# Kernel optimization log

Hardware: AMD Instinct MI355X
Metric: run time of the kernel (lower is better)

The kernel has to match this reference:

```python
import jax, jax.numpy as jnp
import numpy as np

VOCAB = 32000
EMB = 512
T = 20  # sentence_max_length
B = 64


def setup_inputs() -> dict:
    key = jax.random.key(0)
    ks = jax.random.split(key, 8)
    features = jax.random.normal(ks[0], (B, EMB), dtype=jnp.float32)
    captions = jax.random.randint(ks[1], (B, T), 0, VOCAB)
    W_emb = jax.random.normal(ks[2], (VOCAB, EMB), dtype=jnp.float32) * 0.02
    W_out = jax.random.normal(ks[3], (VOCAB, EMB), dtype=jnp.float32) * 0.02
    b_out = jnp.zeros((VOCAB,), dtype=jnp.float32)
    # LSTM params (PyTorch layout: [4*H, in], gate order i, f, g, o)
    W_ih = jax.random.normal(ks[4], (4 * EMB, EMB), dtype=jnp.float32) * (1.0 / np.sqrt(EMB))
    W_hh = jax.random.normal(ks[5], (4 * EMB, EMB), dtype=jnp.float32) * (1.0 / np.sqrt(EMB))
    b_ih = jnp.zeros((4 * EMB,), dtype=jnp.float32)
    b_hh = jnp.zeros((4 * EMB,), dtype=jnp.float32)
    return {"features": features, "captions": captions, "W_emb": W_emb,
            "W_out": W_out, "b_out": b_out, "W_ih": W_ih, "W_hh": W_hh,
            "b_ih": b_ih, "b_hh": b_hh}


def _lstm_scan(emb_steps, h0, c0, W_ih, W_hh, b_ih, b_hh):
    # emb_steps: [T-1, B, E]; returns stacked hidden states [T-1, B, E]
    def cell(carry, x):
        h, c = carry
        gates = x @ W_ih.T + b_ih + h @ W_hh.T + b_hh  # [B, 4E]
        i, f, g, o = jnp.split(gates, 4, axis=-1)
        i, f, o = jax.nn.sigmoid(i), jax.nn.sigmoid(f), jax.nn.sigmoid(o)
        g = jnp.tanh(g)
        c = f * c + i * g
        h = o * jnp.tanh(c)
        return (h, c), h

    (_, _), hs = jax.lax.scan(cell, (h0, c0), emb_steps)
    return hs


def reference(features, captions, W_emb, W_out, b_out, W_ih, W_hh, b_ih, b_hh):
    # Teacher-forced decode. h0 = zeros, c0 = features (per original code).
    emb = W_emb[captions]  # [B, T, E]
    h0 = jnp.zeros_like(features)
    c0 = features
    # Step i (i=1..T-1) consumes embedding of captions[:, i-1]
    xs = jnp.swapaxes(emb[:, : T - 1], 0, 1)  # [T-1, B, E]
    hs = _lstm_scan(xs, h0, c0, W_ih, W_hh, b_ih, b_hh)  # [T-1, B, E]
    hs = jnp.swapaxes(hs, 0, 1)  # [B, T-1, E]
    # out[0] = Linear(Embed(captions[:,0])); out[i] = Linear(h_i)
    seq = jnp.concatenate([emb[:, :1], hs], axis=1)  # [B, T, E]
    logits = jnp.einsum("bte,ve->btv", seq, W_out) + b_out  # [B, T, V]
    return logits
```

## Files before the change

### kernel.cpp

```cpp
#include <hip/hip_runtime.h>
#include <hip/hip_bf16.h>

#define Bb 64
#define Tt 20
#define Ee 512
#define Vv 32000
#define NB 32

typedef __hip_bfloat16 bf16;
typedef __attribute__((ext_vector_type(8))) short bf16x8;
typedef __attribute__((ext_vector_type(4))) float f32x4;

__device__ __forceinline__ bf16 f2bf(float x) { return __float2bfloat16(x); }

__global__ void embed_init(const int* __restrict__ caps, const float* __restrict__ Wemb,
                           bf16* __restrict__ emb, bf16* __restrict__ seq,
                           unsigned int* __restrict__ bar) {
  int row = blockIdx.x;
  int t = row % Tt;
  int tid = threadIdx.x;
  if (row == 0) {
    for (int i = tid; i < NB * 16 + Tt; i += 128) bar[i] = 0;
  }
  int tok = caps[row];
  float4 v = ((const float4*)(Wemb + (size_t)tok * Ee))[tid];
  union { ushort4 u; bf16 h[4]; } pk;
  pk.h[0] = f2bf(v.x); pk.h[1] = f2bf(v.y); pk.h[2] = f2bf(v.z); pk.h[3] = f2bf(v.w);
  ((ushort4*)(emb + (size_t)row * Ee))[tid] = pk.u;
  if (t == 0) ((ushort4*)(seq + (size_t)row * Ee))[tid] = pk.u;
}

__global__ __launch_bounds__(256) void xproj(
    const bf16* __restrict__ A,
    const float* __restrict__ Bw,
    const float* __restrict__ bih, const float* __restrict__ bhh,
    float* __restrict__ gx)
{
  __shared__ __align__(16) bf16 As[128 * 64];
  __shared__ __align__(16) bf16 Bs[128 * 64];
  int tid = threadIdx.x;
  int lane = tid & 63;
  int quad = lane >> 4, ln = lane & 15;
  int wid = tid >> 6;
  int wm = wid & 1, wn = wid >> 1;
  int n0 = blockIdx.x * 128, m0 = blockIdx.y * 128;

  f32x4 zero = {0.f, 0.f, 0.f, 0.f};
  f32x4 acc[4][4];
#pragma unroll
  for (int mt = 0; mt < 4; ++mt)
#pragma unroll
    for (int nt = 0; nt < 4; ++nt) acc[mt][nt] = zero;

  for (int k0 = 0; k0 < Ee; k0 += 64) {
    uint4 avv[4];
    float4 bf0[4], bf1[4];
#pragma unroll
    for (int q = 0; q < 4; ++q) {
      int fb = (q * 256 + tid) * 16;
      int row = fb >> 7;
      int c8 = (fb & 127) >> 1;
      avv[q] = *(const uint4*)((const char*)A + ((size_t)(m0 + row) * Ee + k0) * 2 + (fb & 127));
      const float* src = Bw + (size_t)(n0 + row) * Ee + k0 + c8;
      bf0[q] = *(const float4*)(src);
      bf1[q] = *(const float4*)(src + 4);
    }
#pragma unroll
    for (int q = 0; q < 4; ++q) {
      int fb = (q * 256 + tid) * 16;
      *(uint4*)((char*)As + fb) = avv[q];
      union { uint4 u; bf16 h[8]; } pk;
      pk.h[0] = f2bf(bf0[q].x); pk.h[1] = f2bf(bf0[q].y);
      pk.h[2] = f2bf(bf0[q].z); pk.h[3] = f2bf(bf0[q].w);
      pk.h[4] = f2bf(bf1[q].x); pk.h[5] = f2bf(bf1[q].y);
      pk.h[6] = f2bf(bf1[q].z); pk.h[7] = f2bf(bf1[q].w);
      *(uint4*)((char*)Bs + fb) = pk.u;
    }
    __syncthreads();

#pragma unroll
    for (int kk = 0; kk < 2; ++kk) {
      int kb = (kk * 32 + quad * 8) * 2;
      bf16x8 af[4], bfv[4];
#pragma unroll
      for (int mt = 0; mt < 4; ++mt)
        af[mt] = *(const bf16x8*)((const char*)As + (wm * 64 + mt * 16 + ln) * 128 + kb);
#pragma unroll
      for (int nt = 0; nt < 4; ++nt)
        bfv[nt] = *(const bf16x8*)((const char*)Bs + (wn * 64 + nt * 16 + ln) * 128 + kb);
#pragma unroll
      for (int mt = 0; mt < 4; ++mt)
#pragma unroll
        for (int nt = 0; nt < 4; ++nt)
          acc[mt][nt] = __builtin_amdgcn_mfma_f32_16x16x32_bf16(af[mt], bfv[nt], acc[mt][nt], 0, 0, 0);
    }
    __syncthreads();
  }

#pragma unroll
  for (int nt = 0; nt < 4; ++nt) {
    int col = n0 + wn * 64 + nt * 16 + ln;
    float bsum = bih[col] + bhh[col];
#pragma unroll
    for (int mt = 0; mt < 4; ++mt) {
#pragma unroll
      for (int r = 0; r < 4; ++r) {
        int row = m0 + wm * 64 + mt * 16 + quad * 4 + r;
        gx[(size_t)row * (4 * Ee) + col] = acc[mt][nt][r] + bsum;
      }
    }
  }
}

__global__ __launch_bounds__(256) void lstm_rec(
    const float* __restrict__ gx,
    bf16* __restrict__ seq,
    bf16* __restrict__ hbuf,
    const float* __restrict__ feats,
    const float* __restrict__ Whh,
    unsigned int* __restrict__ bar)
{
  const long XS = (long)Tt * Ee;
  __shared__ __align__(16) bf16 wl[4][64][16][8];
  __shared__ float gsm[4][64][17];

  int tid = threadIdx.x;
  int g = tid >> 6;
  int lane = tid & 63;
  int quad = lane >> 4, ln = lane & 15;
  int j0 = blockIdx.x * 16;
  int bid = blockIdx.x;

#pragma unroll
  for (int q = 0; q < 16; ++q) {
    int c = q * 256 + tid;
    int row = c >> 6, k8 = c & 63;
    int gg = row >> 4, rr = row & 15;
    const float* src = Whh + ((size_t)gg * Ee + j0 + rr) * Ee + k8 * 8;
    float4 f0 = *(const float4*)src;
    float4 f1 = *(const float4*)(src + 4);
    union { uint4 u; bf16 h[8]; } pk;
    pk.h[0] = f2bf(f0.x); pk.h[1] = f2bf(f0.y); pk.h[2] = f2bf(f0.z); pk.h[3] = f2bf(f0.w);
    pk.h[4] = f2bf(f1.x); pk.h[5] = f2bf(f1.y); pk.h[6] = f2bf(f1.z); pk.h[7] = f2bf(f1.w);
    *(uint4*)&wl[gg][k8][rr][0] = pk.u;
  }

  int bq = tid >> 2;
  int jq = (tid & 3) * 4;
  const float* gxb = gx + (size_t)bq * Tt * (4 * Ee) + j0 + jq;

  f32x4 creg = *(const f32x4*)(feats + (size_t)bq * Ee + j0 + jq);

  f32x4 pre[4];
#pragma unroll
  for (int gg = 0; gg < 4; ++gg) pre[gg] = *(const f32x4*)(gxb + gg * Ee);
  __syncthreads();

  for (int t = 1; t < Tt; ++t) {
    if (t > 1) {
      const bf16* hbase = hbuf + (size_t)(t - 1) * NB * 1024;
      f32x4 zero = {0.f, 0.f, 0.f, 0.f};
      f32x4 acc[4];
#pragma unroll
      for (int mt = 0; mt < 4; ++mt) acc[mt] = zero;
#pragma unroll 4
      for (int kk = 0; kk < 16; ++kk) {
        int k = kk * 32 + quad * 8;
        int kb = k >> 4, ko = k & 15;
        bf16x8 bfrag = *(const bf16x8*)&wl[g][kk * 4 + quad][ln][0];
#pragma unroll
        for (int mt = 0; mt < 4; ++mt) {
          bf16x8 afrag = *(const bf16x8*)(hbase + (size_t)kb * 1024 +
                                          (mt * 16 + ln) * 16 + ko);
          acc[mt] = __builtin_amdgcn_mfma_f32_16x16x32_bf16(afrag, bfrag, acc[mt], 0, 0, 0);
        }
      }
#pragma unroll
      for (int mt = 0; mt < 4; ++mt)
#pragma unroll
        for (int r = 0; r < 4; ++r)
          gsm[g][mt * 16 + quad * 4 + r][ln] = acc[mt][r];
    }
    __syncthreads();

    union { ushort4 u; unsigned long long q; bf16 h[4]; } st;
#pragma unroll
    for (int jj = 0; jj < 4; ++jj) {
      int jl = jq + jj;
      float iv = pre[0][jj];
      float fv = pre[1][jj];
      float gv = pre[2][jj];
      float ov = pre[3][jj];
      if (t > 1) {
        iv += gsm[0][bq][jl];
        fv += gsm[1][bq][jl];
        gv += gsm[2][bq][jl];
        ov += gsm[3][bq][jl];
      }
      iv = 1.f / (1.f + __expf(-iv));
      fv = 1.f / (1.f + __expf(-fv));
      ov = 1.f / (1.f + __expf(-ov));
      gv = tanhf(gv);
      creg[jj] = fv * creg[jj] + iv * gv;
      st.h[jj] = f2bf(ov * tanhf(creg[jj]));
    }
    __hip_atomic_store(
        (unsigned long long*)(hbuf + ((size_t)t * NB + bid) * 1024 + bq * 16 + jq),
        st.q, __ATOMIC_RELAXED, __HIP_MEMORY_SCOPE_AGENT);
    *(ushort4*)(seq + (size_t)bq * XS + (size_t)t * Ee + j0 + jq) = st.u;

    if (t < Tt - 1) {
#pragma unroll
      for (int gg = 0; gg < 4; ++gg)
        pre[gg] = *(const f32x4*)(gxb + (size_t)t * (4 * Ee) + gg * Ee);

      __syncthreads();
      if (tid == 0)
        __hip_atomic_store(&bar[bid * 16], (unsigned)t, __ATOMIC_RELAXED,
                           __HIP_MEMORY_SCOPE_AGENT);
      if (tid < NB) {
        while (__hip_atomic_load(&bar[tid * 16], __ATOMIC_RELAXED,
                                 __HIP_MEMORY_SCOPE_AGENT) < (unsigned)t)
          __builtin_amdgcn_s_sleep(1);
      }
      __syncthreads();
    }
  }
}

#define BM 128
#define BN 128
#define BK 64

__global__ __launch_bounds__(256) void out_gemm(const bf16* __restrict__ A,
                                                const float* __restrict__ Bw,
                                                const float* __restrict__ bias,
                                                float* __restrict__ Cb) {
  __shared__ __align__(16) bf16 As[BM * BK];
  __shared__ __align__(16) bf16 Bs[BN * BK];
  int bid = blockIdx.x;
  int xcd = bid & 7, slot = bid >> 3;
  int mi = slot % 10, grp = slot / 10;
  int band = grp * 8 + xcd;
  if (band >= Vv / BN) return;
  int m0 = mi * BM, n0 = band * BN;

  int tid = threadIdx.x;
  int lane = tid & 63;
  int quad = lane >> 4, ln = lane & 15;
  int wid = tid >> 6;
  int wm = wid & 1, wn = wid >> 1;

  f32x4 zero = {0.f, 0.f, 0.f, 0.f};
  f32x4 acc[4][4];
#pragma unroll
  for (int mt = 0; mt < 4; ++mt)
#pragma unroll
    for (int nt = 0; nt < 4; ++nt) acc[mt][nt] = zero;

  for (int k0 = 0; k0 < Ee; k0 += BK) {
    uint4 avv[4];
    float4 bf0[4], bf1[4];
#pragma unroll
    for (int q = 0; q < 4; ++q) {
      int fb = (q * 256 + tid) * 16;
      int row = fb >> 7;
      int c8 = (fb & 127) >> 1;
      avv[q] = *(const uint4*)((const char*)A + ((size_t)(m0 + row) * Ee + k0) * 2 + (fb & 127));
      const float* src = Bw + (size_t)(n0 + row) * Ee + k0 + c8;
      bf0[q] = *(const float4*)(src);
      bf1[q] = *(const float4*)(src + 4);
    }
#pragma unroll
    for (int q = 0; q < 4; ++q) {
      int fb = (q * 256 + tid) * 16;
      *(uint4*)((char*)As + fb) = avv[q];
      union { uint4 u; bf16 h[8]; } pk;
      pk.h[0] = f2bf(bf0[q].x); pk.h[1] = f2bf(bf0[q].y);
      pk.h[2] = f2bf(bf0[q].z); pk.h[3] = f2bf(bf0[q].w);
      pk.h[4] = f2bf(bf1[q].x); pk.h[5] = f2bf(bf1[q].y);
      pk.h[6] = f2bf(bf1[q].z); pk.h[7] = f2bf(bf1[q].w);
      *(uint4*)((char*)Bs + fb) = pk.u;
    }
    __syncthreads();

#pragma unroll
    for (int kk = 0; kk < 2; ++kk) {
      int kb = (kk * 32 + quad * 8) * 2;
      bf16x8 af[4], bfv[4];
#pragma unroll
      for (int mt = 0; mt < 4; ++mt)
        af[mt] = *(const bf16x8*)((const char*)As + (wm * 64 + mt * 16 + ln) * 128 + kb);
#pragma unroll
      for (int nt = 0; nt < 4; ++nt)
        bfv[nt] = *(const bf16x8*)((const char*)Bs + (wn * 64 + nt * 16 + ln) * 128 + kb);
#pragma unroll
      for (int mt = 0; mt < 4; ++mt)
#pragma unroll
        for (int nt = 0; nt < 4; ++nt)
          acc[mt][nt] = __builtin_amdgcn_mfma_f32_16x16x32_bf16(af[mt], bfv[nt], acc[mt][nt], 0, 0, 0);
    }
    __syncthreads();
  }

  float bv[4];
#pragma unroll
  for (int nt = 0; nt < 4; ++nt)
    bv[nt] = bias[n0 + wn * 64 + nt * 16 + ln];
#pragma unroll
  for (int mt = 0; mt < 4; ++mt) {
#pragma unroll
    for (int nt = 0; nt < 4; ++nt) {
      int col = n0 + wn * 64 + nt * 16 + ln;
#pragma unroll
      for (int r = 0; r < 4; ++r) {
        int row = m0 + wm * 64 + mt * 16 + quad * 4 + r;
        Cb[(size_t)row * Vv + col] = acc[mt][nt][r] + bv[nt];
      }
    }
  }
}

extern "C" void kernel_launch(void* const* d_in, const int* in_sizes, int n_in,
                              void* d_out, int out_size, void* d_ws, size_t ws_size,
                              hipStream_t stream) {
  (void)in_sizes; (void)n_in; (void)out_size; (void)ws_size;
  const float* feats = (const float*)d_in[0];
  const int*   caps  = (const int*)d_in[1];
  const float* Wemb  = (const float*)d_in[2];
  const float* Wout  = (const float*)d_in[3];
  const float* bout  = (const float*)d_in[4];
  const float* Wih   = (const float*)d_in[5];
  const float* Whh   = (const float*)d_in[6];
  const float* bih   = (const float*)d_in[7];
  const float* bhh   = (const float*)d_in[8];
  float* out = (float*)d_out;

  bf16* emb    = (bf16*)d_ws;
  bf16* seq    = emb   + (size_t)Bb * Tt * Ee;
  bf16* hbuf   = seq   + (size_t)Bb * Tt * Ee;
  float* gx    = (float*)(hbuf + (size_t)Tt * NB * 1024);
  unsigned int* bar = (unsigned int*)(gx + (size_t)Bb * Tt * 4 * Ee);

  embed_init<<<Bb * Tt, 128, 0, stream>>>(caps, Wemb, emb, seq, bar);
  xproj<<<dim3(16, 10), 256, 0, stream>>>(emb, Wih, bih, bhh, gx);
  lstm_rec<<<NB, 256, 0, stream>>>(gx, seq, hbuf, feats, Whh, bar);
  out_gemm<<<2560, 256, 0, stream>>>(seq, Wout, bout, out);
}
```

Measured before the change: 520.5 us.

## Co-locate LSTM recurrence blocks on one XCD and use plain L2-scoped sync

Launches 256 blocks for the recurrence kernel. Blocks on XCC 0 claim the 32 work slots first through an atomic ticket, while blocks on other dies sleep before claiming. When all claimed slots land on the same die, the h-state stores and the grid barrier switch from agent-scope atomics to plain volatile accesses, so they can stay in the shared L2 and skip cross-die coherence. This adds startup sleep and ticket overhead. It also relies on hardware scheduling and on volatile accesses staying coherent within one XCD.

```diff
diff --git a/kernel.cpp b/kernel.cpp
--- a/kernel.cpp
+++ b/kernel.cpp
@@ -20,7 +20,7 @@
   int t = row % Tt;
   int tid = threadIdx.x;
   if (row == 0) {
-    for (int i = tid; i < NB * 16 + Tt; i += 128) bar[i] = 0;
+    for (int i = tid; i < 640; i += 128) bar[i] = 0;
   }
   int tok = caps[row];
   float4 v = ((const float4*)(Wemb + (size_t)tok * Ee))[tid];
@@ -123,13 +123,34 @@
   const long XS = (long)Tt * Ee;
   __shared__ __align__(16) bf16 wl[4][64][16][8];
   __shared__ float gsm[4][64][17];
+  __shared__ int s_slot, s_fast;
 
   int tid = threadIdx.x;
   int g = tid >> 6;
   int lane = tid & 63;
   int quad = lane >> 4, ln = lane & 15;
-  int j0 = blockIdx.x * 16;
-  int bid = blockIdx.x;
+
+  int xcc;
+  asm volatile("s_getreg_b32 %0, hwreg(HW_REG_XCC_ID)" : "=s"(xcc));
+  xcc &= 15;
+
+  if (tid == 0) {
+    if (xcc != 0) {
+#pragma unroll 1
+      for (int i = 0; i < 8; ++i) __builtin_amdgcn_s_sleep(127);
+    }
+    int sl = (int)__hip_atomic_fetch_add(&bar[512], 1u, __ATOMIC_RELAXED,
+                                         __HIP_MEMORY_SCOPE_AGENT);
+    s_slot = sl;
+    if (sl < NB)
+      __hip_atomic_store(&bar[528 + sl], (unsigned)(xcc + 1), __ATOMIC_RELAXED,
+                         __HIP_MEMORY_SCOPE_AGENT);
+  }
+  __syncthreads();
+  int slot = s_slot;
+  if (slot >= NB) return;
+  int bid = slot;
+  int j0 = slot * 16;
 
 #pragma unroll
   for (int q = 0; q < 16; ++q) {
@@ -154,7 +175,22 @@
   f32x4 pre[4];
 #pragma unroll
   for (int gg = 0; gg < 4; ++gg) pre[gg] = *(const f32x4*)(gxb + gg * Ee);
+
+  if (tid < 64) {
+    unsigned v = 0;
+    if (tid < NB) {
+      do {
+        v = __hip_atomic_load(&bar[528 + tid], __ATOMIC_RELAXED,
+                              __HIP_MEMORY_SCOPE_AGENT);
+      } while (v == 0);
+    }
+    unsigned v0 = __shfl(v, 0);
+    int ok = (tid < NB) ? (v == v0) : 1;
+    int fast = __all(ok);
+    if (tid == 0) s_fast = fast;
+  }
   __syncthreads();
+  int fastmode = s_fast;
 
   for (int t = 1; t < Tt; ++t) {
     if (t > 1) {
@@ -204,9 +240,13 @@
       creg[jj] = fv * creg[jj] + iv * gv;
       st.h[jj] = f2bf(ov * tanhf(creg[jj]));
     }
-    __hip_atomic_store(
-        (unsigned long long*)(hbuf + ((size_t)t * NB + bid) * 1024 + bq * 16 + jq),
-        st.q, __ATOMIC_RELAXED, __HIP_MEMORY_SCOPE_AGENT);
+    unsigned long long* hdst =
+        (unsigned long long*)(hbuf + ((size_t)t * NB + bid) * 1024 + bq * 16 + jq);
+    if (fastmode) {
+      *hdst = st.q;
+    } else {
+      __hip_atomic_store(hdst, st.q, __ATOMIC_RELAXED, __HIP_MEMORY_SCOPE_AGENT);
+    }
     *(ushort4*)(seq + (size_t)bq * XS + (size_t)t * Ee + j0 + jq) = st.u;
 
     if (t < Tt - 1) {
@@ -215,13 +255,22 @@
         pre[gg] = *(const f32x4*)(gxb + (size_t)t * (4 * Ee) + gg * Ee);
 
       __syncthreads();
-      if (tid == 0)
-        __hip_atomic_store(&bar[bid * 16], (unsigned)t, __ATOMIC_RELAXED,
-                           __HIP_MEMORY_SCOPE_AGENT);
-      if (tid < NB) {
-        while (__hip_atomic_load(&bar[tid * 16], __ATOMIC_RELAXED,
-                                 __HIP_MEMORY_SCOPE_AGENT) < (unsigned)t)
-          __builtin_amdgcn_s_sleep(1);
+      if (fastmode) {
+        if (tid == 0)
+          *(volatile unsigned*)&bar[bid * 16] = (unsigned)t;
+        if (tid < NB) {
+          while (*(volatile unsigned*)&bar[tid * 16] < (unsigned)t)
+            __builtin_amdgcn_s_sleep(1);
+        }
+      } else {
+        if (tid == 0)
+          __hip_atomic_store(&bar[bid * 16], (unsigned)t, __ATOMIC_RELAXED,
+                             __HIP_MEMORY_SCOPE_AGENT);
+        if (tid < NB) {
+          while (__hip_atomic_load(&bar[tid * 16], __ATOMIC_RELAXED,
+                                   __HIP_MEMORY_SCOPE_AGENT) < (unsigned)t)
+            __builtin_amdgcn_s_sleep(1);
+        }
       }
       __syncthreads();
     }
@@ -344,6 +393,6 @@
 
   embed_init<<<Bb * Tt, 128, 0, stream>>>(caps, Wemb, emb, seq, bar);
   xproj<<<dim3(16, 10), 256, 0, stream>>>(emb, Wih, bih, bhh, gx);
-  lstm_rec<<<NB, 256, 0, stream>>>(gx, seq, hbuf, feats, Whh, bar);
+  lstm_rec<<<256, 256, 0, stream>>>(gx, seq, hbuf, feats, Whh, bar);
   out_gemm<<<2560, 256, 0, stream>>>(seq, Wout, bout, out);
 }
```

Measured after the change: 610.4 us. +17.3%, slower.
